# Kernel tuning notes

Hardware: AMD Instinct MI355X
Metric: run time of the kernel (lower is better)

## Reference

```python
import jax, jax.numpy as jnp
import numpy as np

B = 256
THRESH = 0.0
SHIFT = 0.0


def setup_inputs() -> dict:
    key = jax.random.key(0)
    ks = jax.random.split(key, 8)
    s = lambda k, shape, sc: (jax.random.normal(k, shape, jnp.float32) * sc)
    return {
        "x": jax.random.normal(ks[0], (B, 3, 250, 250), jnp.float32),
        "conv1_w": s(ks[1], (6, 3, 5, 5), 0.08),
        "conv1_b": jnp.zeros((6,), jnp.float32),
        "conv2_w": s(ks[2], (15, 6, 3, 3), 0.12),
        "conv2_b": jnp.zeros((15,), jnp.float32),
        "fc1_w": s(ks[3], (120, 55815), 0.004),
        "fc1_b": jnp.zeros((120,), jnp.float32),
        "fc2_w": s(ks[4], (84, 120), 0.09),
        "fc2_b": jnp.zeros((84,), jnp.float32),
        "fc3_w": s(ks[5], (1, 84), 0.1),
        "fc3_b": jnp.zeros((1,), jnp.float32),
        "pl_w": s(ks[6], (1, 1), 1.0),
        "pl_b": jnp.zeros((1,), jnp.float32),
        "pl_scale": jnp.ones((1,), jnp.float32),
        "pl_bias": jnp.zeros((1,), jnp.float32),
    }


def _conv2d(x, w, b, stride, pad):
    y = jax.lax.conv_general_dilated(
        x, w, (stride, stride), [(pad, pad), (pad, pad)],
        dimension_numbers=("NCHW", "OIHW", "NCHW"))
    return y + b[None, :, None, None]


def _maxpool_k2_s1(x):
    return jax.lax.reduce_window(x, -jnp.inf, jax.lax.max,
                                 (1, 1, 2, 2), (1, 1, 1, 1), "VALID")


def reference(x, conv1_w, conv1_b, conv2_w, conv2_b, fc1_w, fc1_b,
              fc2_w, fc2_b, fc3_w, fc3_b, pl_w, pl_b, pl_scale, pl_bias):
    # CNN backbone (dropout layers are eval-mode no-ops)
    h = jax.nn.relu(_conv2d(x, conv1_w, conv1_b, 2, 1))   # [B,6,124,124]
    h = _maxpool_k2_s1(h)                                  # [B,6,123,123]
    h = jax.nn.relu(_conv2d(h, conv2_w, conv2_b, 2, 1))   # [B,15,62,62]
    h = _maxpool_k2_s1(h)                                  # [B,15,61,61]
    h = h.reshape(h.shape[0], -1)                          # [B,55815]
    h = jax.nn.relu(h @ fc1_w.T + fc1_b)                   # [B,120]
    features = h @ fc2_w.T + fc2_b                         # [B,84]

    # head: fc3 -> ParameterizedLayer -> sigmoid
    logits = features @ fc3_w.T + fc3_b                    # [B,1]
    z = jnp.tanh(logits @ pl_w.T + pl_b) * pl_scale + pl_bias + SHIFT
    probs = jax.nn.sigmoid(z)[:, 0]                        # [B]

    # dynamic cosine-similarity graph (fidelity_adjacency, secondary=None)
    norms = jnp.linalg.norm(features, axis=1)              # [B]
    sim = (features @ features.T) / (norms[:, None] * norms[None, :] + 1e-12)
    adj = (sim >= THRESH) & (~jnp.eye(features.shape[0], dtype=bool))
    adjf = adj.astype(probs.dtype)                         # [B,B] 0/1

    # degree-weighted neighbor-mean aggregation
    deg = adjf.sum(axis=1)                                 # [B]
    neigh_mean = jnp.where(deg > 0, (adjf @ probs) / jnp.maximum(deg, 1.0), 0.0)
    agg = (probs + neigh_mean) / (1.0 + deg)
    return jnp.stack([agg, 1.0 - agg], axis=-1)            # [B,2]
```

## Files before the change

### kernel.cpp

```cpp
#include <hip/hip_runtime.h>
#include <math.h>


__global__ __launch_bounds__(256) void k_c1p1(const float* __restrict__ x,
                                              const float* __restrict__ w,
                                              const float* __restrict__ bias,
                                              float* __restrict__ p1) {
    __shared__ float xs[22][258];

    const int t    = blockIdx.x;
    const int b    = blockIdx.y;
    const int tid  = threadIdx.x;
    const int lane = tid & 63;
    const int wv   = tid >> 6;
    const int s    = wv & 1;
    const int q    = wv >> 1;
    const int ow   = 62 * s + lane;
    const int owc  = min(ow, 123);
    const int owc2 = 2 * owc;
    const int ihlo = 16 * t - 1;

    const int sr  = __builtin_amdgcn_readfirstlane(tid >> 7);
    const int sm  = tid & 127;
    const int smc = min(sm, 124);

    float acc[5][6];
#pragma unroll
    for (int j = 0; j < 5; ++j)
#pragma unroll
        for (int oc = 0; oc < 6; ++oc) acc[j][oc] = 0.f;

    const float* xb = x + (size_t)b * 3 * 62500;

#pragma unroll 1
    for (int ci = 0; ci < 3; ++ci) {
        __syncthreads();
        const float* xc = xb + (size_t)ci * 62500;
        float2 vv[11];
#pragma unroll
        for (int i = 0; i < 11; ++i) {
            int r   = 2 * i + sr;
            int ih  = ihlo + r;
            int ihc = min(max(ih, 0), 249);
            bool ok = (ih >= 0) && (ih < 250);
            float2 raw = *(const float2*)(xc + (size_t)ihc * 250 + (smc << 1));
            vv[i].x = ok ? raw.x : 0.f;
            vv[i].y = ok ? raw.y : 0.f;
        }
#pragma unroll
        for (int i = 0; i < 11; ++i) {
            int r = 2 * i + sr;
            xs[r][2 * sm + 1] = vv[i].x;
            xs[r][2 * sm + 2] = vv[i].y;
        }
        if (tid < 21) xs[tid][0] = 0.f;
        __syncthreads();

        float rr[7][5];
#pragma unroll
        for (int t7 = 0; t7 < 7; ++t7) {
            const float* pp = &xs[8 * q + 2 * t7][owc2];
            rr[t7][0] = pp[0]; rr[t7][1] = pp[1]; rr[t7][2] = pp[2];
            rr[t7][3] = pp[3]; rr[t7][4] = pp[4];
        }
#pragma unroll
        for (int kp = 0; kp < 3; ++kp) {
            const int kh = 2 * kp;
            float wk[6][5];
#pragma unroll
            for (int oc = 0; oc < 6; ++oc)
#pragma unroll
                for (int kw = 0; kw < 5; ++kw)
                    wk[oc][kw] = w[((oc * 3 + ci) * 5 + kh) * 5 + kw];
#pragma unroll
            for (int j = 0; j < 5; ++j) {
                const float* rp = rr[j + kp];
#pragma unroll
                for (int oc = 0; oc < 6; ++oc) {
                    float a = acc[j][oc];
                    a = fmaf(rp[0], wk[oc][0], a);
                    a = fmaf(rp[1], wk[oc][1], a);
                    a = fmaf(rp[2], wk[oc][2], a);
                    a = fmaf(rp[3], wk[oc][3], a);
                    a = fmaf(rp[4], wk[oc][4], a);
                    acc[j][oc] = a;
                }
            }
        }
#pragma unroll
        for (int t6 = 0; t6 < 6; ++t6) {
            const float* pp = &xs[8 * q + 2 * t6 + 1][owc2];
            rr[t6][0] = pp[0]; rr[t6][1] = pp[1]; rr[t6][2] = pp[2];
            rr[t6][3] = pp[3]; rr[t6][4] = pp[4];
        }
#pragma unroll
        for (int kp = 0; kp < 2; ++kp) {
            const int kh = 2 * kp + 1;
            float wk[6][5];
#pragma unroll
            for (int oc = 0; oc < 6; ++oc)
#pragma unroll
                for (int kw = 0; kw < 5; ++kw)
                    wk[oc][kw] = w[((oc * 3 + ci) * 5 + kh) * 5 + kw];
#pragma unroll
            for (int j = 0; j < 5; ++j) {
                const float* rp = rr[j + kp];
#pragma unroll
                for (int oc = 0; oc < 6; ++oc) {
                    float a = acc[j][oc];
                    a = fmaf(rp[0], wk[oc][0], a);
                    a = fmaf(rp[1], wk[oc][1], a);
                    a = fmaf(rp[2], wk[oc][2], a);
                    a = fmaf(rp[3], wk[oc][3], a);
                    a = fmaf(rp[4], wk[oc][4], a);
                    acc[j][oc] = a;
                }
            }
        }
    }

    const int pw   = ow;
    const int oh0  = 8 * t + 4 * q;
    const bool cok = (lane < 63) && (pw < 123);
#pragma unroll
    for (int oc = 0; oc < 6; ++oc) {
        float bv = bias[oc];
        float r0 = fmaxf(acc[0][oc] + bv, 0.f);
        float r1 = fmaxf(acc[1][oc] + bv, 0.f);
        float r2 = fmaxf(acc[2][oc] + bv, 0.f);
        float r3 = fmaxf(acc[3][oc] + bv, 0.f);
        float r4 = fmaxf(acc[4][oc] + bv, 0.f);
        float vm0 = fmaxf(r0, r1), vm1 = fmaxf(r1, r2);
        float vm2 = fmaxf(r2, r3), vm3 = fmaxf(r3, r4);
        float p0 = fmaxf(vm0, __shfl_down(vm0, 1));
        float p1v = fmaxf(vm1, __shfl_down(vm1, 1));
        float p2v = fmaxf(vm2, __shfl_down(vm2, 1));
        float p3 = fmaxf(vm3, __shfl_down(vm3, 1));
        if (cok) {
            float* op = p1 + (((size_t)b * 6 + oc) * 123) * 123 + pw;
            if (oh0 + 0 < 123) op[(size_t)(oh0 + 0) * 123] = p0;
            if (oh0 + 1 < 123) op[(size_t)(oh0 + 1) * 123] = p1v;
            if (oh0 + 2 < 123) op[(size_t)(oh0 + 2) * 123] = p2v;
            if (oh0 + 3 < 123) op[(size_t)(oh0 + 3) * 123] = p3;
        }
    }
}

__global__ __launch_bounds__(256) void k_c2p2(const float* __restrict__ p1,
                                              const float* __restrict__ w,
                                              const float* __restrict__ bias,
                                              float* __restrict__ p2) {
    __shared__ float xs[20][130];

    const int v    = blockIdx.x;
    const int b    = blockIdx.y;
    const int tid  = threadIdx.x;
    const int lane = tid & 63;
    const int q    = tid >> 6;
    const int ow   = lane;
    const int owc  = min(ow, 61);
    const int owc2 = 2 * owc;
    const int ihlo = 16 * v - 1;

    const int sr   = __builtin_amdgcn_readfirstlane(tid >> 7);
    const int sc   = tid & 127;
    const int scc  = min(sc, 122);
    const int wcol = (sc < 123) ? (sc + 1) : 129;

    float acc[3][15];
#pragma unroll
    for (int j = 0; j < 3; ++j)
#pragma unroll
        for (int oc = 0; oc < 15; ++oc) acc[j][oc] = 0.f;

    const float* ib = p1 + (size_t)b * 6 * 15129;

#pragma unroll 1
    for (int ci = 0; ci < 6; ++ci) {
        __syncthreads();
        const float* xc = ib + (size_t)ci * 15129;
        float vv[10];
#pragma unroll
        for (int i = 0; i < 10; ++i) {
            int r   = 2 * i + sr;
            int ih  = ihlo + r;
            int ihc = min(max(ih, 0), 122);
            bool ok = (ih >= 0) && (ih < 123);
            float raw = xc[(size_t)ihc * 123 + scc];
            vv[i] = ok ? raw : 0.f;
        }
#pragma unroll
        for (int i = 0; i < 10; ++i) {
            int r = 2 * i + sr;
            xs[r][wcol] = vv[i];
        }
        if (tid < 19) { xs[tid][0] = 0.f; xs[tid][124] = 0.f; }
        __syncthreads();

        float rr[7][3];
#pragma unroll
        for (int c = 0; c < 7; ++c) {
            const float* pp = &xs[4 * q + c][owc2];
            rr[c][0] = pp[0]; rr[c][1] = pp[1]; rr[c][2] = pp[2];
        }
#pragma unroll
        for (int kh = 0; kh < 3; ++kh) {
            float wk[15][3];
#pragma unroll
            for (int oc = 0; oc < 15; ++oc)
#pragma unroll
                for (int kw = 0; kw < 3; ++kw)
                    wk[oc][kw] = w[((oc * 6 + ci) * 3 + kh) * 3 + kw];
#pragma unroll
            for (int j = 0; j < 3; ++j) {
                const float* rp = rr[2 * j + kh];
#pragma unroll
                for (int oc = 0; oc < 15; ++oc) {
                    float a = acc[j][oc];
                    a = fmaf(rp[0], wk[oc][0], a);
                    a = fmaf(rp[1], wk[oc][1], a);
                    a = fmaf(rp[2], wk[oc][2], a);
                    acc[j][oc] = a;
                }
            }
        }
    }

    const int pw   = ow;
    const int oh0  = 8 * v + 2 * q;
    const bool cok = (lane < 61);
#pragma unroll
    for (int oc = 0; oc < 15; ++oc) {
        float bv = bias[oc];
        float r0 = fmaxf(acc[0][oc] + bv, 0.f);
        float r1 = fmaxf(acc[1][oc] + bv, 0.f);
        float r2 = fmaxf(acc[2][oc] + bv, 0.f);
        float vm0 = fmaxf(r0, r1), vm1 = fmaxf(r1, r2);
        float p0 = fmaxf(vm0, __shfl_down(vm0, 1));
        float p1v = fmaxf(vm1, __shfl_down(vm1, 1));
        if (cok) {
            float* op = p2 + (((size_t)b * 15 + oc) * 61) * 61 + pw;
            if (oh0 + 0 < 61) op[(size_t)(oh0 + 0) * 61] = p0;
            if (oh0 + 1 < 61) op[(size_t)(oh0 + 1) * 61] = p1v;
        }
    }
}

__global__ __launch_bounds__(256) void k_fc1(const float* __restrict__ A,
                                             const float* __restrict__ B,
                                             float* __restrict__ partial) {
    __shared__ float As[128][64];
    __shared__ float Bs[128][64];
    const int K = 55815;
    int tid = threadIdx.x;
    int kb  = blockIdx.x;
    int m0  = blockIdx.y * 128;
    int mx  = tid >> 4;
    int nx  = tid & 15;
    int kl  = tid & 63;
    int mb  = tid >> 6;

    Bs[120 + mb][kl] = 0.f;
    Bs[124 + mb][kl] = 0.f;

    float acc[8][8];
#pragma unroll
    for (int i = 0; i < 8; ++i)
#pragma unroll
        for (int j = 0; j < 8; ++j) acc[i][j] = 0.f;

    for (int ch = kb; ch < 873; ch += 256) {
        int k    = ch * 64 + kl;
        bool kok = (k < K);
        int kc   = kok ? k : K - 1;
        __syncthreads();
#pragma unroll
        for (int batch = 0; batch < 4; ++batch) {
            float va[8], vb[8];
#pragma unroll
            for (int u = 0; u < 8; ++u) {
                int m = mb + 4 * (batch * 8 + u);
                va[u] = A[(size_t)(m0 + m) * K + kc];
            }
#pragma unroll
            for (int u = 0; u < 8; ++u) {
                if (batch < 3 || u < 6) {
                    int m = mb + 4 * (batch * 8 + u);
                    vb[u] = B[(size_t)m * K + kc];
                }
            }
#pragma unroll
            for (int u = 0; u < 8; ++u) {
                int m = mb + 4 * (batch * 8 + u);
                As[m][kl ^ ((m & 7) << 2)] = kok ? va[u] : 0.f;
            }
#pragma unroll
            for (int u = 0; u < 8; ++u) {
                if (batch < 3 || u < 6) {
                    int m = mb + 4 * (batch * 8 + u);
                    Bs[m][kl ^ ((m & 7) << 2)] = kok ? vb[u] : 0.f;
                }
            }
        }
        __syncthreads();
#pragma unroll 2
        for (int k4 = 0; k4 < 16; ++k4) {
            float4 af[8], bf[8];
#pragma unroll
            for (int i = 0; i < 8; ++i) {
                int m = mx + 16 * i;
                af[i] = *(const float4*)&As[m][(k4 * 4) ^ ((m & 7) << 2)];
            }
#pragma unroll
            for (int j = 0; j < 8; ++j) {
                int n = nx + 16 * j;
                bf[j] = *(const float4*)&Bs[n][(k4 * 4) ^ ((n & 7) << 2)];
            }
#pragma unroll
            for (int i = 0; i < 8; ++i)
#pragma unroll
                for (int j = 0; j < 8; ++j) {
                    acc[i][j] = fmaf(af[i].x, bf[j].x, acc[i][j]);
                    acc[i][j] = fmaf(af[i].y, bf[j].y, acc[i][j]);
                    acc[i][j] = fmaf(af[i].z, bf[j].z, acc[i][j]);
                    acc[i][j] = fmaf(af[i].w, bf[j].w, acc[i][j]);
                }
        }
    }

    float* pp = partial + (size_t)kb * 30720;
#pragma unroll
    for (int i = 0; i < 8; ++i) {
        int m = m0 + mx + 16 * i;
#pragma unroll
        for (int j = 0; j < 8; ++j) {
            int n = nx + 16 * j;
            if (n < 120) pp[m * 120 + n] = acc[i][j];
        }
    }
}

__global__ __launch_bounds__(256) void k_fc1red(const float* __restrict__ partial,
                                                const float* __restrict__ bias,
                                                float* __restrict__ out) {
    int idx = blockIdx.x * 256 + threadIdx.x;
    int n = idx % 120;
    float s = bias[n];
#pragma unroll 8
    for (int kb = 0; kb < 256; ++kb) s += partial[(size_t)kb * 30720 + idx];
    out[idx] = fmaxf(s, 0.f);
}

__global__ __launch_bounds__(256) void k_fc2(const float* __restrict__ h,
                                             const float* __restrict__ w,
                                             const float* __restrict__ bias,
                                             float* __restrict__ out) {
    int idx = blockIdx.x * 256 + threadIdx.x;
    int n = idx % 84;
    int m = idx / 84;
    const float* hp = h + m * 120;
    const float* wp = w + n * 120;
    float s = bias[n];
#pragma unroll 4
    for (int k = 0; k < 120; ++k) s = fmaf(hp[k], wp[k], s);
    out[idx] = s;
}

__global__ __launch_bounds__(256) void k_head(const float* __restrict__ f,
                                              const float* __restrict__ w3,
                                              const float* __restrict__ b3,
                                              const float* __restrict__ plw,
                                              const float* __restrict__ plb,
                                              const float* __restrict__ pls,
                                              const float* __restrict__ plbias,
                                              float* __restrict__ probs,
                                              float* __restrict__ norms) {
    int b = threadIdx.x;
    const float* fp = f + b * 84;
    float nsq = 0.f, lg = b3[0];
#pragma unroll 4
    for (int k = 0; k < 84; ++k) {
        float v = fp[k];
        nsq = fmaf(v, v, nsq);
        lg  = fmaf(v, w3[k], lg);
    }
    float z = tanhf(lg * plw[0] + plb[0]) * pls[0] + plbias[0];
    probs[b] = 1.f / (1.f + expf(-z));
    norms[b] = sqrtf(nsq);
}

__global__ __launch_bounds__(256) void k_graph(const float* __restrict__ f,
                                               const float* __restrict__ probs,
                                               const float* __restrict__ norms,
                                               float* __restrict__ out) {
    __shared__ float fi[84];
    __shared__ float sd[4], sv[4];
    int i = blockIdx.x;
    int j = threadIdx.x;
    if (j < 84) fi[j] = f[i * 84 + j];
    __syncthreads();
    const float* fj = f + j * 84;
    float dot = 0.f;
#pragma unroll 4
    for (int k = 0; k < 84; ++k) dot = fmaf(fi[k], fj[k], dot);
    float sim = dot / (norms[i] * norms[j] + 1e-12f);
    bool adj = (j != i) && (sim >= 0.0f);
    float d = adj ? 1.f : 0.f;
    float v = adj ? probs[j] : 0.f;
#pragma unroll
    for (int off = 32; off >= 1; off >>= 1) {
        d += __shfl_down(d, off);
        v += __shfl_down(v, off);
    }
    int wave = j >> 6, lane = j & 63;
    if (lane == 0) { sd[wave] = d; sv[wave] = v; }
    __syncthreads();
    if (j == 0) {
        float D = sd[0] + sd[1] + sd[2] + sd[3];
        float V = sv[0] + sv[1] + sv[2] + sv[3];
        float nm = (D > 0.f) ? (V / fmaxf(D, 1.f)) : 0.f;
        float agg = (probs[i] + nm) / (1.f + D);
        out[2 * i]     = agg;
        out[2 * i + 1] = 1.f - agg;
    }
}

extern "C" void kernel_launch(void* const* d_in, const int* in_sizes, int n_in,
                              void* d_out, int out_size, void* d_ws, size_t ws_size,
                              hipStream_t stream) {
    const float* x    = (const float*)d_in[0];
    const float* w1   = (const float*)d_in[1];
    const float* b1   = (const float*)d_in[2];
    const float* w2   = (const float*)d_in[3];
    const float* b2   = (const float*)d_in[4];
    const float* fw1  = (const float*)d_in[5];
    const float* fb1  = (const float*)d_in[6];
    const float* fw2  = (const float*)d_in[7];
    const float* fb2  = (const float*)d_in[8];
    const float* fw3  = (const float*)d_in[9];
    const float* fb3  = (const float*)d_in[10];
    const float* plw  = (const float*)d_in[11];
    const float* plb  = (const float*)d_in[12];
    const float* pls  = (const float*)d_in[13];
    const float* plbi = (const float*)d_in[14];
    float* out = (float*)d_out;

    float* ws = (float*)d_ws;
    float* p1       = ws;
    float* p2       = p1 + 23238144;
    float* partial  = p2 + 14288640;
    float* fc1out   = partial + 7864320;
    float* features = fc1out + 30720;
    float* probs    = features + 21504;
    float* norms    = probs + 256;

    k_c1p1<<<dim3(16, 256), 256, 0, stream>>>(x, w1, b1, p1);
    k_c2p2<<<dim3(8, 256), 256, 0, stream>>>(p1, w2, b2, p2);
    k_fc1<<<dim3(256, 2), 256, 0, stream>>>(p2, fw1, partial);
    k_fc1red<<<120, 256, 0, stream>>>(partial, fb1, fc1out);
    k_fc2<<<84, 256, 0, stream>>>(fc1out, fw2, fb2, features);
    k_head<<<1, 256, 0, stream>>>(features, fw3, fb3, plw, plb, pls, plbi,
                                  probs, norms);
    k_graph<<<256, 256, 0, stream>>>(features, probs, norms, out);
}
```

Measured before the change: 488.3 us.

## Split fc1 reduction into two stages, merge conv1 row loads, set min-blocks hints

The fc1 partial-sum reduction, which ran 256 serial loads per thread on only 120 blocks, is split into a 960-block first stage over 32-slice groups and a small second stage that adds bias and ReLU. This spreads the 31 MB read of partial sums across many more CUs. The conv1 kernel now loads all 13 input rows into registers once instead of doing separate even and odd row passes. Conv1 and conv2 also get a min-blocks-per-CU launch bound of 3, which caps register use and may cause spills.

```diff
diff --git a/kernel.cpp b/kernel.cpp
--- a/kernel.cpp
+++ b/kernel.cpp
@@ -2,10 +2,10 @@
 #include <math.h>
 
 
-__global__ __launch_bounds__(256) void k_c1p1(const float* __restrict__ x,
-                                              const float* __restrict__ w,
-                                              const float* __restrict__ bias,
-                                              float* __restrict__ p1) {
+__global__ __launch_bounds__(256, 3) void k_c1p1(const float* __restrict__ x,
+                                                 const float* __restrict__ w,
+                                                 const float* __restrict__ bias,
+                                                 float* __restrict__ p1) {
     __shared__ float xs[22][258];
 
     const int t    = blockIdx.x;
@@ -56,16 +56,15 @@
         if (tid < 21) xs[tid][0] = 0.f;
         __syncthreads();
 
-        float rr[7][5];
-#pragma unroll
-        for (int t7 = 0; t7 < 7; ++t7) {
-            const float* pp = &xs[8 * q + 2 * t7][owc2];
-            rr[t7][0] = pp[0]; rr[t7][1] = pp[1]; rr[t7][2] = pp[2];
-            rr[t7][3] = pp[3]; rr[t7][4] = pp[4];
-        }
-#pragma unroll
-        for (int kp = 0; kp < 3; ++kp) {
-            const int kh = 2 * kp;
+        float rr[13][5];
+#pragma unroll
+        for (int r = 0; r < 13; ++r) {
+            const float* pp = &xs[8 * q + r][owc2];
+            rr[r][0] = pp[0]; rr[r][1] = pp[1]; rr[r][2] = pp[2];
+            rr[r][3] = pp[3]; rr[r][4] = pp[4];
+        }
+#pragma unroll
+        for (int kh = 0; kh < 5; ++kh) {
             float wk[6][5];
 #pragma unroll
             for (int oc = 0; oc < 6; ++oc)
@@ -74,37 +73,7 @@
                     wk[oc][kw] = w[((oc * 3 + ci) * 5 + kh) * 5 + kw];
 #pragma unroll
             for (int j = 0; j < 5; ++j) {
-                const float* rp = rr[j + kp];
-#pragma unroll
-                for (int oc = 0; oc < 6; ++oc) {
-                    float a = acc[j][oc];
-                    a = fmaf(rp[0], wk[oc][0], a);
-                    a = fmaf(rp[1], wk[oc][1], a);
-                    a = fmaf(rp[2], wk[oc][2], a);
-                    a = fmaf(rp[3], wk[oc][3], a);
-                    a = fmaf(rp[4], wk[oc][4], a);
-                    acc[j][oc] = a;
-                }
-            }
-        }
-#pragma unroll
-        for (int t6 = 0; t6 < 6; ++t6) {
-            const float* pp = &xs[8 * q + 2 * t6 + 1][owc2];
-            rr[t6][0] = pp[0]; rr[t6][1] = pp[1]; rr[t6][2] = pp[2];
-            rr[t6][3] = pp[3]; rr[t6][4] = pp[4];
-        }
-#pragma unroll
-        for (int kp = 0; kp < 2; ++kp) {
-            const int kh = 2 * kp + 1;
-            float wk[6][5];
-#pragma unroll
-            for (int oc = 0; oc < 6; ++oc)
-#pragma unroll
-                for (int kw = 0; kw < 5; ++kw)
-                    wk[oc][kw] = w[((oc * 3 + ci) * 5 + kh) * 5 + kw];
-#pragma unroll
-            for (int j = 0; j < 5; ++j) {
-                const float* rp = rr[j + kp];
+                const float* rp = rr[2 * j + kh];
 #pragma unroll
                 for (int oc = 0; oc < 6; ++oc) {
                     float a = acc[j][oc];
@@ -146,10 +115,10 @@
     }
 }
 
-__global__ __launch_bounds__(256) void k_c2p2(const float* __restrict__ p1,
-                                              const float* __restrict__ w,
-                                              const float* __restrict__ bias,
-                                              float* __restrict__ p2) {
+__global__ __launch_bounds__(256, 3) void k_c2p2(const float* __restrict__ p1,
+                                                 const float* __restrict__ w,
+                                                 const float* __restrict__ bias,
+                                                 float* __restrict__ p2) {
     __shared__ float xs[20][130];
 
     const int v    = blockIdx.x;
@@ -340,14 +309,25 @@
     }
 }
 
-__global__ __launch_bounds__(256) void k_fc1red(const float* __restrict__ partial,
-                                                const float* __restrict__ bias,
-                                                float* __restrict__ out) {
+__global__ __launch_bounds__(256) void k_fc1red1(const float* __restrict__ partial,
+                                                 float* __restrict__ partial2) {
+    int idx = blockIdx.x * 256 + threadIdx.x;
+    int s   = blockIdx.y;
+    const float* p = partial + (size_t)(s * 32) * 30720 + idx;
+    float acc = 0.f;
+#pragma unroll 8
+    for (int kb = 0; kb < 32; ++kb) acc += p[(size_t)kb * 30720];
+    partial2[(size_t)s * 30720 + idx] = acc;
+}
+
+__global__ __launch_bounds__(256) void k_fc1red2(const float* __restrict__ partial2,
+                                                 const float* __restrict__ bias,
+                                                 float* __restrict__ out) {
     int idx = blockIdx.x * 256 + threadIdx.x;
     int n = idx % 120;
     float s = bias[n];
-#pragma unroll 8
-    for (int kb = 0; kb < 256; ++kb) s += partial[(size_t)kb * 30720 + idx];
+#pragma unroll
+    for (int k = 0; k < 8; ++k) s += partial2[(size_t)k * 30720 + idx];
     out[idx] = fmaxf(s, 0.f);
 }
 
@@ -453,11 +433,13 @@
     float* features = fc1out + 30720;
     float* probs    = features + 21504;
     float* norms    = probs + 256;
+    float* partial2 = norms + 256;
 
     k_c1p1<<<dim3(16, 256), 256, 0, stream>>>(x, w1, b1, p1);
     k_c2p2<<<dim3(8, 256), 256, 0, stream>>>(p1, w2, b2, p2);
     k_fc1<<<dim3(256, 2), 256, 0, stream>>>(p2, fw1, partial);
-    k_fc1red<<<120, 256, 0, stream>>>(partial, fb1, fc1out);
+    k_fc1red1<<<dim3(120, 8), 256, 0, stream>>>(partial, partial2);
+    k_fc1red2<<<120, 256, 0, stream>>>(partial2, fb1, fc1out);
     k_fc2<<<84, 256, 0, stream>>>(fc1out, fw2, fb2, features);
     k_head<<<1, 256, 0, stream>>>(features, fw3, fb3, plw, plb, pls, plbi,
                                   probs, norms);
```

After: 488.2 us. No clear change (-0.0%).
